# Kernel tuning notes

Hardware: AMD Instinct MI355X
Metric: run time of the kernel (lower is better)

Reference implementation:

```python
import jax, jax.numpy as jnp
import numpy as np

B, S, D, H, DK, DV = 4, 1024, 1024, 16, 64, 64
NEG = jnp.float32(-1e10)


def setup_inputs() -> dict:
    key = jax.random.key(0)
    ks = jax.random.split(key, 9)
    q = jax.random.normal(ks[0], (B, S, D), dtype=jnp.float32)
    k = jax.random.normal(ks[1], (B, S, D), dtype=jnp.float32)
    v = jax.random.normal(ks[2], (B, S, D), dtype=jnp.float32)
    pad_mask_1 = jax.random.randint(ks[3], (B,), 1, S + 1, dtype=jnp.int32)
    pad_mask_2 = jax.random.randint(ks[4], (B,), 1, S + 1, dtype=jnp.int32)
    # Per-head projection weights stacked over heads (torch Linear, bias=False).
    sc = 1.0 / np.sqrt(D)
    Wq = jax.random.uniform(ks[5], (H, D, DK), jnp.float32, -sc, sc)
    Wk = jax.random.uniform(ks[6], (H, D, DK), jnp.float32, -sc, sc)
    Wv = jax.random.uniform(ks[7], (H, D, DV), jnp.float32, -sc, sc)
    Wo = jax.random.uniform(ks[8], (H * DV, D), jnp.float32, -sc, sc)
    return {"q": q, "k": k, "v": v, "pad_mask_1": pad_mask_1,
            "pad_mask_2": pad_mask_2, "Wq": Wq, "Wk": Wk, "Wv": Wv, "Wo": Wo}


def reference(q, k, v, pad_mask_1, pad_mask_2, Wq, Wk, Wv, Wo):
    Bq, Sq, _ = q.shape
    scale = jnp.sqrt(jnp.float32(Wq.shape[-1]))
    qh = jnp.einsum('bsd,hdk->bhsk', q, Wq)   # [B,H,S,DK]
    kh = jnp.einsum('bsd,hdk->bhsk', k, Wk)
    vh = jnp.einsum('bsd,hdv->bhsv', v, Wv)
    w = jnp.einsum('bhqk,bhtk->bhqt', qh, kh) / scale  # [B,H,S,S]
    idx = jnp.arange(Sq)
    # pad_mask_1: mask key columns >= length; pad_mask_2: mask query rows >= length
    key_dead = idx[None, :] >= pad_mask_1[:, None]      # [B,S]
    row_dead = idx[None, :] >= pad_mask_2[:, None]      # [B,S]
    w = jnp.where(key_dead[:, None, None, :], NEG, w)
    w = jnp.where(row_dead[:, None, :, None], NEG, w)
    # causal: w.tril() + (-1e10).triu(1) == keep lower triangle, NEG strictly above
    causal = idx[None, :] > idx[:, None]                # [S,S] strictly upper
    w = jnp.where(causal[None, None], NEG, w)
    a = jax.nn.softmax(w, axis=-1)
    o = jnp.einsum('bhqt,bhtv->bhqv', a, vh)            # [B,H,S,DV]
    o = o.transpose(0, 2, 1, 3).reshape(Bq, Sq, -1)     # concat heads (head-major)
    return o @ Wo
```

## Files before the change

### kernel.cpp

```cpp
#include <hip/hip_runtime.h>

#define B_ 4
#define S_ 1024
#define D_ 1024
#define H_ 16
#define BSD (B_*S_*D_)

typedef unsigned short ushort_t;
typedef __attribute__((ext_vector_type(8))) __bf16 bf16x8;
typedef __attribute__((ext_vector_type(8))) ushort_t ushortx8;
typedef __attribute__((ext_vector_type(4))) float f32x4;

__device__ __forceinline__ ushort_t f2bf(float f) {
  union { float f; unsigned int u; } x; x.f = f;
  unsigned int r = x.u + 0x7fffu + ((x.u >> 16) & 1u);
  return (ushort_t)(r >> 16);
}

__device__ __forceinline__ void gll16(const void* g, void* l) {
  __builtin_amdgcn_global_load_lds(
      (const __attribute__((address_space(1))) unsigned int*)g,
      (__attribute__((address_space(3))) unsigned int*)l, 16, 0, 0);
}

#define PBAR() do { asm volatile("s_waitcnt lgkmcnt(0)" ::: "memory"); \
                    __builtin_amdgcn_s_barrier(); \
                    asm volatile("" ::: "memory"); } while (0)

__global__ __launch_bounds__(256) void transpose_w(
    const float* __restrict__ Wq, const float* __restrict__ Wk,
    const float* __restrict__ Wv, const float* __restrict__ Wo,
    ushort_t* __restrict__ WqT, ushort_t* __restrict__ WkT,
    ushort_t* __restrict__ WvT, ushort_t* __restrict__ WoT)
{
  __shared__ float tile[64][65];
  int blk = blockIdx.x;
  const float* src; ushort_t* dst;
  size_t sbase, dbase; int ld_src, ld_dst, r0, c0;
  if (blk < 768) {
    int tz = blk / 256;
    int rem = blk % 256; int head = rem >> 4; int kt = rem & 15;
    src = (tz == 0) ? Wq : (tz == 1) ? Wk : Wv;
    dst = (tz == 0) ? WqT : (tz == 1) ? WkT : WvT;
    sbase = (size_t)head * 1024 * 64; dbase = (size_t)head * 64 * 1024;
    ld_src = 64; ld_dst = 1024; r0 = kt * 64; c0 = 0;
  } else {
    int idx = blk - 768; src = Wo; dst = WoT;
    sbase = 0; dbase = 0; ld_src = 1024; ld_dst = 1024;
    r0 = (idx >> 4) * 64; c0 = (idx & 15) * 64;
  }
  int tid = threadIdx.x; int col = tid & 63; int rbase = tid >> 6;
  #pragma unroll
  for (int j = 0; j < 16; ++j) {
    int row = j * 4 + rbase;
    tile[row][col] = src[sbase + (size_t)(r0 + row) * ld_src + c0 + col];
  }
  __syncthreads();
  #pragma unroll
  for (int j = 0; j < 16; ++j) {
    int orow = j * 4 + rbase;
    dst[dbase + (size_t)(c0 + orow) * ld_dst + r0 + col] = f2bf(tile[col][orow]);
  }
}

__device__ __forceinline__ void gemm_pipe_f32A(
    const float* __restrict__ Af, const ushort_t* __restrict__ BT,
    ushort_t* __restrict__ Cb, int epi, int m0, int n0, int K)
{
  __shared__ __align__(16) ushort_t As[2][128 * 64];
  __shared__ __align__(16) ushort_t Bs[2][128 * 64];
  const int tid = threadIdx.x;
  const int wave = tid >> 6, lane = tid & 63;
  const int wm = wave >> 2, wn = wave & 3;

  f32x4 acc[4][2] = {};
  float4   ra0[2][2], ra1[2][2];
  ushortx8 rb0[2],    rb1[2];

  int offs[2], gofs[2];
  #pragma unroll
  for (int i = 0; i < 2; ++i) {
    int off = ((i * 8 + wave) << 10) + lane * 16;
    int row = off >> 7, cb = off & 127;
    int lcb = cb ^ ((row & 7) << 4);
    offs[i] = off;
    gofs[i] = row * K + (lcb >> 1);
  }

  auto loadAB = [&](float4 (&ar)[2][2], ushortx8 (&br)[2], int k0) {
    #pragma unroll
    for (int i = 0; i < 2; ++i) {
      const float* asrc = Af + (size_t)m0 * K + gofs[i] + k0;
      ar[i][0] = *(const float4*)(asrc);
      ar[i][1] = *(const float4*)(asrc + 4);
      br[i] = *(const ushortx8*)(BT + (size_t)n0 * K + gofs[i] + k0);
    }
  };
  auto writeAB = [&](int buf, const float4 (&ar)[2][2], const ushortx8 (&br)[2]) {
    #pragma unroll
    for (int i = 0; i < 2; ++i) {
      ushortx8 tv;
      #pragma unroll
      for (int j = 0; j < 4; ++j) {
        tv[j]     = f2bf(((const float*)&ar[i][0])[j]);
        tv[4 + j] = f2bf(((const float*)&ar[i][1])[j]);
      }
      *(ushortx8*)((char*)As[buf] + offs[i]) = tv;
      *(ushortx8*)((char*)Bs[buf] + offs[i]) = br[i];
    }
  };
  auto compute = [&](int buf) {
    #pragma unroll
    for (int kk = 0; kk < 2; ++kk) {
      bf16x8 af[4], bfr[2];
      #pragma unroll
      for (int mf = 0; mf < 4; ++mf) {
        int row = wm * 64 + mf * 16 + (lane & 15);
        int cb = kk * 64 + ((lane >> 4) << 4);
        af[mf] = *(const bf16x8*)((const char*)As[buf] + (row << 7) + (cb ^ ((row & 7) << 4)));
      }
      #pragma unroll
      for (int nf = 0; nf < 2; ++nf) {
        int row = wn * 32 + nf * 16 + (lane & 15);
        int cb = kk * 64 + ((lane >> 4) << 4);
        bfr[nf] = *(const bf16x8*)((const char*)Bs[buf] + (row << 7) + (cb ^ ((row & 7) << 4)));
      }
      #pragma unroll
      for (int mf = 0; mf < 4; ++mf)
        #pragma unroll
        for (int nf = 0; nf < 2; ++nf)
          acc[mf][nf] = __builtin_amdgcn_mfma_f32_16x16x32_bf16(af[mf], bfr[nf], acc[mf][nf], 0, 0, 0);
    }
  };

  const int nt = K >> 6;
  loadAB(ra0, rb0, 0);
  writeAB(0, ra0, rb0);
  loadAB(ra1, rb1, 64);
  PBAR();

  for (int t = 0; t < nt - 3; t += 2) {
    loadAB(ra0, rb0, (t + 2) << 6);
    __builtin_amdgcn_sched_barrier(0);
    compute(0);
    writeAB(1, ra1, rb1);
    PBAR();
    loadAB(ra1, rb1, (t + 3) << 6);
    __builtin_amdgcn_sched_barrier(0);
    compute(1);
    writeAB(0, ra0, rb0);
    PBAR();
  }
  compute(0);
  writeAB(1, ra1, rb1);
  PBAR();
  compute(1);

  #pragma unroll
  for (int mf = 0; mf < 4; ++mf) {
    #pragma unroll
    for (int nf = 0; nf < 2; ++nf) {
      #pragma unroll
      for (int r = 0; r < 4; ++r) {
        int m = m0 + wm * 64 + mf * 16 + ((lane >> 4) << 2) + r;
        int n = n0 + wn * 32 + nf * 16 + (lane & 15);
        float val = acc[mf][nf][r];
        if (epi == 0) {
          int b = m >> 10, s = m & 1023, h = n >> 6, dk = n & 63;
          Cb[((((size_t)(b * H_ + h)) << 10) + s) * 64 + dk] = f2bf(val);
        } else {
          int b = m >> 10, s = m & 1023, h = n >> 6, dv = n & 63;
          Cb[((((size_t)(b * H_ + h)) * 64 + dv) << 10) + s] = f2bf(val);
        }
      }
    }
  }
}

__device__ __forceinline__ void gemm_pipe_bf16(
    const ushort_t* __restrict__ A, const ushort_t* __restrict__ BT,
    float* __restrict__ Cf, int m0, int n0, int K)
{
  __shared__ __align__(16) ushort_t As[2][128 * 64];
  __shared__ __align__(16) ushort_t Bs[2][128 * 64];
  const int tid = threadIdx.x;
  const int wave = tid >> 6, lane = tid & 63;
  const int wm = wave >> 2, wn = wave & 3;

  f32x4 acc[4][2] = {};
  ushortx8 ra0[2], ra1[2], rb0[2], rb1[2];

  int offs[2], gofs[2];
  #pragma unroll
  for (int i = 0; i < 2; ++i) {
    int off = ((i * 8 + wave) << 10) + lane * 16;
    int row = off >> 7, cb = off & 127;
    int lcb = cb ^ ((row & 7) << 4);
    offs[i] = off;
    gofs[i] = row * K + (lcb >> 1);
  }

  auto loadAB = [&](ushortx8 (&ar)[2], ushortx8 (&br)[2], int k0) {
    #pragma unroll
    for (int i = 0; i < 2; ++i) {
      ar[i] = *(const ushortx8*)(A  + (size_t)m0 * K + gofs[i] + k0);
      br[i] = *(const ushortx8*)(BT + (size_t)n0 * K + gofs[i] + k0);
    }
  };
  auto writeAB = [&](int buf, const ushortx8 (&ar)[2], const ushortx8 (&br)[2]) {
    #pragma unroll
    for (int i = 0; i < 2; ++i) {
      *(ushortx8*)((char*)As[buf] + offs[i]) = ar[i];
      *(ushortx8*)((char*)Bs[buf] + offs[i]) = br[i];
    }
  };
  auto compute = [&](int buf) {
    #pragma unroll
    for (int kk = 0; kk < 2; ++kk) {
      bf16x8 af[4], bfr[2];
      #pragma unroll
      for (int mf = 0; mf < 4; ++mf) {
        int row = wm * 64 + mf * 16 + (lane & 15);
        int cb = kk * 64 + ((lane >> 4) << 4);
        af[mf] = *(const bf16x8*)((const char*)As[buf] + (row << 7) + (cb ^ ((row & 7) << 4)));
      }
      #pragma unroll
      for (int nf = 0; nf < 2; ++nf) {
        int row = wn * 32 + nf * 16 + (lane & 15);
        int cb = kk * 64 + ((lane >> 4) << 4);
        bfr[nf] = *(const bf16x8*)((const char*)Bs[buf] + (row << 7) + (cb ^ ((row & 7) << 4)));
      }
      #pragma unroll
      for (int mf = 0; mf < 4; ++mf)
        #pragma unroll
        for (int nf = 0; nf < 2; ++nf)
          acc[mf][nf] = __builtin_amdgcn_mfma_f32_16x16x32_bf16(af[mf], bfr[nf], acc[mf][nf], 0, 0, 0);
    }
  };

  const int nt = K >> 6;
  loadAB(ra0, rb0, 0);
  writeAB(0, ra0, rb0);
  loadAB(ra1, rb1, 64);
  PBAR();

  for (int t = 0; t < nt - 3; t += 2) {
    loadAB(ra0, rb0, (t + 2) << 6);
    __builtin_amdgcn_sched_barrier(0);
    compute(0);
    writeAB(1, ra1, rb1);
    PBAR();
    loadAB(ra1, rb1, (t + 3) << 6);
    __builtin_amdgcn_sched_barrier(0);
    compute(1);
    writeAB(0, ra0, rb0);
    PBAR();
  }
  compute(0);
  writeAB(1, ra1, rb1);
  PBAR();
  compute(1);

  #pragma unroll
  for (int mf = 0; mf < 4; ++mf) {
    #pragma unroll
    for (int nf = 0; nf < 2; ++nf) {
      #pragma unroll
      for (int r = 0; r < 4; ++r) {
        int m = m0 + wm * 64 + mf * 16 + ((lane >> 4) << 2) + r;
        int n = n0 + wn * 32 + nf * 16 + (lane & 15);
        Cf[(size_t)m * 1024 + n] = acc[mf][nf][r];
      }
    }
  }
}

__global__ __launch_bounds__(512, 4) void proj_gemm(
    const float* q, const float* k, const float* v,
    const ushort_t* WqT, const ushort_t* WkT, const ushort_t* WvT,
    ushort_t* qh, ushort_t* kh, ushort_t* vhT)
{
  int f = blockIdx.x;
  int xcd = f & 7;
  int slot = f >> 3;
  int g = xcd * 12 + (slot >> 3);
  int y = slot & 7;
  int z = g >> 5, x = g & 31;
  const float* A = (z == 0) ? q : (z == 1) ? k : v;
  const ushort_t* BT = (z == 0) ? WqT : (z == 1) ? WkT : WvT;
  ushort_t* C = (z == 0) ? qh : (z == 1) ? kh : vhT;
  gemm_pipe_f32A(A, BT, C, (z == 2) ? 1 : 0, x * 128, y * 128, 1024);
}

__global__ __launch_bounds__(512, 4) void out_gemm(
    const ushort_t* o, const ushort_t* WoT, float* out)
{
  int f = blockIdx.x;
  int xcd = f & 7;
  int slot = f >> 3;
  int x = xcd * 4 + (slot >> 3);
  int y = slot & 7;
  gemm_pipe_bf16(o, WoT, out, x * 128, y * 128, 1024);
}

__global__ __launch_bounds__(256) void meanv_kernel(
    const ushort_t* __restrict__ vhT, float* __restrict__ meanV)
{
  int row = blockIdx.x * 4 + (threadIdx.x >> 6);
  int lane = threadIdx.x & 63;
  const ushort_t* src = vhT + ((size_t)row << 10) + lane * 16;
  float s = 0.f;
  #pragma unroll
  for (int i = 0; i < 2; ++i) {
    bf16x8 v = *(const bf16x8*)(src + i * 8);
    #pragma unroll
    for (int j = 0; j < 8; ++j) s += (float)v[j];
  }
  #pragma unroll
  for (int mm = 1; mm < 64; mm <<= 1) s += __shfl_xor(s, mm);
  if (lane == 0) meanV[row] = s * (1.0f / 1024.0f);
}

__global__ __launch_bounds__(256) void attn_kernel(
    const ushort_t* __restrict__ qh, const ushort_t* __restrict__ kh,
    const ushort_t* __restrict__ vhT, const float* __restrict__ meanV,
    const int* __restrict__ pad1p, const int* __restrict__ pad2p,
    ushort_t* __restrict__ o)
{
  const int bh = blockIdx.x;
  const int b = bh >> 4, h = bh & 15;
  const int q0 = blockIdx.y << 6;
  const int pad1 = pad1p[b], pad2 = pad2p[b];
  const int tid = threadIdx.x, wave = tid >> 6, lane = tid & 63;

  if (q0 >= pad2) {
    int dv = tid & 63;
    int rw = tid >> 6;
    ushort_t mb = f2bf(meanV[(bh << 6) + dv]);
    for (int r = rw; r < 64; r += 4)
      o[(((size_t)((b << 10) + q0 + r)) << 10) + (h << 6) + dv] = mb;
    return;
  }

  __shared__ __align__(16) ushort_t Ks[64 * 64];
  __shared__ __align__(16) ushort_t Vs[64 * 64];
  __shared__ __align__(16) ushort_t Ps[4][16 * 64];

  const ushort_t* qbase = qh + ((size_t)bh << 16);
  const ushort_t* kbase = kh + ((size_t)bh << 16);
  const ushort_t* vbase = vhT + ((size_t)bh << 16);

  const int qrow = q0 + wave * 16 + (lane & 15);
  bf16x8 qf[2];
  qf[0] = *(const bf16x8*)(qbase + (size_t)qrow * 64 + ((lane >> 4) << 3));
  qf[1] = *(const bf16x8*)(qbase + (size_t)qrow * 64 + 32 + ((lane >> 4) << 3));

  f32x4 acc[4] = {};
  float mrow[4] = { -1e30f, -1e30f, -1e30f, -1e30f };
  float lrow[4] = { 0.f, 0.f, 0.f, 0.f };
  const int ribase = q0 + wave * 16 + ((lane >> 4) << 2);

  int t_hi = min(q0 + 63, min(pad2 - 1, pad1 - 1));
  int nb = (t_hi >> 6) + 1;

  for (int kb = 0; kb < nb; ++kb) {
    const int t0 = kb << 6;
    #pragma unroll
    for (int i = 0; i < 2; ++i) {
      int off = ((i * 4 + wave) << 10) + lane * 16;
      int row = off >> 7;
      int cb = off & 127;
      int lcb = cb ^ ((row & 7) << 4);
      gll16(kbase + (size_t)(t0 + row) * 64 + (lcb >> 1), (char*)Ks + off);
      gll16(vbase + ((size_t)row << 10) + t0 + (lcb >> 1), (char*)Vs + off);
    }
    __syncthreads();

    f32x4 sc[4];
    #pragma unroll
    for (int nf = 0; nf < 4; ++nf) {
      sc[nf] = (f32x4){0.f, 0.f, 0.f, 0.f};
      #pragma unroll
      for (int kk = 0; kk < 2; ++kk) {
        int trow = nf * 16 + (lane & 15);
        int cb = kk * 64 + ((lane >> 4) << 4);
        bf16x8 kf = *(const bf16x8*)((const char*)Ks + (trow << 7) + (cb ^ ((trow & 7) << 4)));
        sc[nf] = __builtin_amdgcn_mfma_f32_16x16x32_bf16(qf[kk], kf, sc[nf], 0, 0, 0);
      }
    }

    float pv[4][4];
    #pragma unroll
    for (int r = 0; r < 4; ++r) {
      const int irow = ribase + r;
      float sval[4];
      float rmax = -1e30f;
      #pragma unroll
      for (int nf = 0; nf < 4; ++nf) {
        int t = t0 + nf * 16 + (lane & 15);
        float vv = sc[nf][r] * 0.125f;
        if (t > irow || t >= pad1) vv = -1e10f;
        sval[nf] = vv;
        rmax = fmaxf(rmax, vv);
      }
      #pragma unroll
      for (int mm = 1; mm < 16; mm <<= 1) rmax = fmaxf(rmax, __shfl_xor(rmax, mm));
      float nm = fmaxf(mrow[r], rmax);
      float fscale = __expf(mrow[r] - nm);
      float rsum = 0.f;
      #pragma unroll
      for (int nf = 0; nf < 4; ++nf) {
        float p = __expf(sval[nf] - nm);
        pv[nf][r] = p;
        rsum += p;
      }
      #pragma unroll
      for (int mm = 1; mm < 16; mm <<= 1) rsum += __shfl_xor(rsum, mm);
      mrow[r] = nm;
      lrow[r] = lrow[r] * fscale + rsum;
      #pragma unroll
      for (int dvf = 0; dvf < 4; ++dvf) acc[dvf][r] *= fscale;
    }

    #pragma unroll
    for (int nf = 0; nf < 4; ++nf) {
      #pragma unroll
      for (int r = 0; r < 4; ++r) {
        int prow = ((lane >> 4) << 2) + r;
        int cbw = (nf * 16 + (lane & 15)) * 2;
        *(ushort_t*)((char*)Ps[wave] + (prow << 7) + (cbw ^ ((prow & 7) << 4))) = f2bf(pv[nf][r]);
      }
    }

    #pragma unroll
    for (int kk = 0; kk < 2; ++kk) {
      int prow = lane & 15;
      int cb = kk * 64 + ((lane >> 4) << 4);
      bf16x8 pf = *(const bf16x8*)((const char*)Ps[wave] + (prow << 7) + (cb ^ ((prow & 7) << 4)));
      #pragma unroll
      for (int dvf = 0; dvf < 4; ++dvf) {
        int vrow = dvf * 16 + (lane & 15);
        bf16x8 vfr = *(const bf16x8*)((const char*)Vs + (vrow << 7) + (cb ^ ((vrow & 7) << 4)));
        acc[dvf] = __builtin_amdgcn_mfma_f32_16x16x32_bf16(pf, vfr, acc[dvf], 0, 0, 0);
      }
    }
    __syncthreads();
  }

  #pragma unroll
  for (int dvf = 0; dvf < 4; ++dvf) {
    #pragma unroll
    for (int r = 0; r < 4; ++r) {
      int irow = ribase + r;
      int dv = dvf * 16 + (lane & 15);
      float val;
      if (irow < pad2) val = acc[dvf][r] * (1.0f / lrow[r]);
      else val = meanV[(bh << 6) + dv];
      o[(((size_t)((b << 10) + irow)) << 10) + (h << 6) + dv] = f2bf(val);
    }
  }
}

extern "C" void kernel_launch(void* const* d_in, const int* in_sizes, int n_in,
                              void* d_out, int out_size, void* d_ws, size_t ws_size,
                              hipStream_t stream) {
  (void)in_sizes; (void)n_in; (void)out_size; (void)ws_size;
  const float* q = (const float*)d_in[0];
  const float* k = (const float*)d_in[1];
  const float* v = (const float*)d_in[2];
  const int* pad1 = (const int*)d_in[3];
  const int* pad2 = (const int*)d_in[4];
  const float* Wq = (const float*)d_in[5];
  const float* Wk = (const float*)d_in[6];
  const float* Wv = (const float*)d_in[7];
  const float* Wo = (const float*)d_in[8];
  float* out = (float*)d_out;

  char* ws = (char*)d_ws;
  const size_t MB = 1u << 20;
  ushort_t* WqT = (ushort_t*)(ws + 24 * MB);
  ushort_t* WkT = (ushort_t*)(ws + 26 * MB);
  ushort_t* WvT = (ushort_t*)(ws + 28 * MB);
  ushort_t* WoT = (ushort_t*)(ws + 30 * MB);
  ushort_t* qh  = (ushort_t*)(ws + 32 * MB);
  ushort_t* kh  = (ushort_t*)(ws + 40 * MB);
  ushort_t* vhT = (ushort_t*)(ws + 48 * MB);
  ushort_t* ob  = (ushort_t*)(ws + 56 * MB);
  float* meanV  = (float*)(ws + 64 * MB);

  transpose_w<<<1024, 256, 0, stream>>>(Wq, Wk, Wv, Wo, WqT, WkT, WvT, WoT);
  proj_gemm<<<768, 512, 0, stream>>>(q, k, v, WqT, WkT, WvT, qh, kh, vhT);
  meanv_kernel<<<1024, 256, 0, stream>>>(vhT, meanV);
  attn_kernel<<<dim3(64, 16), 256, 0, stream>>>(qh, kh, vhT, meanV, pad1, pad2, ob);
  out_gemm<<<256, 512, 0, stream>>>(ob, WoT, out);
}
```

Baseline: 99.02 us.

## Shrink projection GEMM tile to 128x64, single-buffer LDS, stage B via direct-to-LDS loads

The projection GEMM is rewritten as a standalone kernel with a 128x64 output tile, twice as many blocks, a single LDS buffer and a higher occupancy bound (512 threads, 8 blocks). The weight operand is copied straight into LDS with global_load_lds instead of passing through registers, while the fp32 activations are still converted to bf16 in registers. The aim is more resident waves and lower register and LDS pressure to hide memory latency. In exchange it drops double buffering, adds two barriers per k-step, and re-reads the fp32 A operand twice as often across blocks.

```diff
diff --git a/kernel.cpp b/kernel.cpp
--- a/kernel.cpp
+++ b/kernel.cpp
@@ -63,9 +63,134 @@
   }
 }
 
-__device__ __forceinline__ void gemm_pipe_f32A(
-    const float* __restrict__ Af, const ushort_t* __restrict__ BT,
-    ushort_t* __restrict__ Cb, int epi, int m0, int n0, int K)
+__global__ __launch_bounds__(512, 8) void proj_gemm(
+    const float* __restrict__ q, const float* __restrict__ k,
+    const float* __restrict__ v,
+    const ushort_t* __restrict__ WqT, const ushort_t* __restrict__ WkT,
+    const ushort_t* __restrict__ WvT,
+    ushort_t* __restrict__ qh, ushort_t* __restrict__ kh,
+    ushort_t* __restrict__ vhT)
+{
+  const int f = blockIdx.x;
+  const int xcd = f & 7;
+  const int slot = f >> 3;
+  const int combo = xcd * 12 + (slot >> 4);
+  const int y = slot & 15;
+  const int z = combo >> 5, x = combo & 31;
+  const float* Af = (z == 0) ? q : (z == 1) ? k : v;
+  const ushort_t* BT = (z == 0) ? WqT : (z == 1) ? WkT : WvT;
+  ushort_t* Cb = (z == 0) ? qh : (z == 1) ? kh : vhT;
+  const int epi = (z == 2) ? 1 : 0;
+  const int m0 = x * 128, n0 = y * 64;
+  const int K = 1024;
+
+  __shared__ __align__(16) ushort_t As[128 * 64];
+  __shared__ __align__(16) ushort_t Bs[64 * 64];
+  const int tid = threadIdx.x;
+  const int wave = tid >> 6, lane = tid & 63;
+  const int wm = wave >> 1, wn = wave & 1;
+
+  f32x4 acc[2][2] = {};
+  float4 ra[2][2];
+
+  int offA[2], gofA[2];
+  #pragma unroll
+  for (int i = 0; i < 2; ++i) {
+    int off = ((i * 8 + wave) << 10) + lane * 16;
+    int row = off >> 7, cb = off & 127;
+    int lcb = cb ^ ((row & 7) << 4);
+    offA[i] = off; gofA[i] = row * K + (lcb >> 1);
+  }
+  const int offB = (wave << 10) + lane * 16;
+  const int rowB = offB >> 7, cbB = offB & 127;
+  const int gofB = rowB * K + ((cbB ^ ((rowB & 7) << 4)) >> 1);
+
+  auto loadA = [&](int k0) {
+    #pragma unroll
+    for (int i = 0; i < 2; ++i) {
+      const float* s = Af + (size_t)m0 * K + gofA[i] + k0;
+      ra[i][0] = *(const float4*)(s);
+      ra[i][1] = *(const float4*)(s + 4);
+    }
+  };
+  auto writeA = [&]() {
+    #pragma unroll
+    for (int i = 0; i < 2; ++i) {
+      ushortx8 tv;
+      #pragma unroll
+      for (int j = 0; j < 4; ++j) {
+        tv[j]     = f2bf(((const float*)&ra[i][0])[j]);
+        tv[4 + j] = f2bf(((const float*)&ra[i][1])[j]);
+      }
+      *(ushortx8*)((char*)As + offA[i]) = tv;
+    }
+  };
+  auto stageB = [&](int k0) {
+    gll16(BT + (size_t)n0 * K + gofB + k0, (char*)Bs + offB);
+  };
+  auto compute = [&]() {
+    #pragma unroll
+    for (int kk = 0; kk < 2; ++kk) {
+      bf16x8 af[2], bfr[2];
+      #pragma unroll
+      for (int mf = 0; mf < 2; ++mf) {
+        int row = wm * 32 + mf * 16 + (lane & 15);
+        int cb = kk * 64 + ((lane >> 4) << 4);
+        af[mf] = *(const bf16x8*)((const char*)As + (row << 7) + (cb ^ ((row & 7) << 4)));
+      }
+      #pragma unroll
+      for (int nf = 0; nf < 2; ++nf) {
+        int row = wn * 32 + nf * 16 + (lane & 15);
+        int cb = kk * 64 + ((lane >> 4) << 4);
+        bfr[nf] = *(const bf16x8*)((const char*)Bs + (row << 7) + (cb ^ ((row & 7) << 4)));
+      }
+      #pragma unroll
+      for (int mf = 0; mf < 2; ++mf)
+        #pragma unroll
+        for (int nf = 0; nf < 2; ++nf)
+          acc[mf][nf] = __builtin_amdgcn_mfma_f32_16x16x32_bf16(af[mf], bfr[nf], acc[mf][nf], 0, 0, 0);
+    }
+  };
+
+  loadA(0);
+  stageB(0);
+  writeA();
+  __syncthreads();
+
+  for (int t = 0; t < 15; ++t) {
+    loadA((t + 1) << 6);
+    compute();
+    __syncthreads();
+    writeA();
+    stageB((t + 1) << 6);
+    __syncthreads();
+  }
+  compute();
+
+  #pragma unroll
+  for (int mf = 0; mf < 2; ++mf) {
+    #pragma unroll
+    for (int nf = 0; nf < 2; ++nf) {
+      #pragma unroll
+      for (int r = 0; r < 4; ++r) {
+        int m = m0 + wm * 32 + mf * 16 + ((lane >> 4) << 2) + r;
+        int n = n0 + wn * 32 + nf * 16 + (lane & 15);
+        float val = acc[mf][nf][r];
+        if (epi == 0) {
+          int b = m >> 10, s = m & 1023, h = n >> 6, dk = n & 63;
+          Cb[((((size_t)(b * H_ + h)) << 10) + s) * 64 + dk] = f2bf(val);
+        } else {
+          int b = m >> 10, s = m & 1023, h = n >> 6, dv = n & 63;
+          Cb[((((size_t)(b * H_ + h)) * 64 + dv) << 10) + s] = f2bf(val);
+        }
+      }
+    }
+  }
+}
+
+__device__ __forceinline__ void gemm_pipe_bf16(
+    const ushort_t* __restrict__ A, const ushort_t* __restrict__ BT,
+    float* __restrict__ Cf, int m0, int n0, int K)
 {
   __shared__ __align__(16) ushort_t As[2][128 * 64];
   __shared__ __align__(16) ushort_t Bs[2][128 * 64];
@@ -74,8 +199,7 @@
   const int wm = wave >> 2, wn = wave & 3;
 
   f32x4 acc[4][2] = {};
-  float4   ra0[2][2], ra1[2][2];
-  ushortx8 rb0[2],    rb1[2];
+  ushortx8 ra0[2], ra1[2], rb0[2], rb1[2];
 
   int offs[2], gofs[2];
   #pragma unroll
@@ -87,25 +211,17 @@
     gofs[i] = row * K + (lcb >> 1);
   }
 
-  auto loadAB = [&](float4 (&ar)[2][2], ushortx8 (&br)[2], int k0) {
+  auto loadAB = [&](ushortx8 (&ar)[2], ushortx8 (&br)[2], int k0) {
     #pragma unroll
     for (int i = 0; i < 2; ++i) {
-      const float* asrc = Af + (size_t)m0 * K + gofs[i] + k0;
-      ar[i][0] = *(const float4*)(asrc);
-      ar[i][1] = *(const float4*)(asrc + 4);
+      ar[i] = *(const ushortx8*)(A  + (size_t)m0 * K + gofs[i] + k0);
       br[i] = *(const ushortx8*)(BT + (size_t)n0 * K + gofs[i] + k0);
     }
   };
-  auto writeAB = [&](int buf, const float4 (&ar)[2][2], const ushortx8 (&br)[2]) {
+  auto writeAB = [&](int buf, const ushortx8 (&ar)[2], const ushortx8 (&br)[2]) {
     #pragma unroll
     for (int i = 0; i < 2; ++i) {
-      ushortx8 tv;
-      #pragma unroll
-      for (int j = 0; j < 4; ++j) {
-        tv[j]     = f2bf(((const float*)&ar[i][0])[j]);
-        tv[4 + j] = f2bf(((const float*)&ar[i][1])[j]);
-      }
-      *(ushortx8*)((char*)As[buf] + offs[i]) = tv;
+      *(ushortx8*)((char*)As[buf] + offs[i]) = ar[i];
       *(ushortx8*)((char*)Bs[buf] + offs[i]) = br[i];
     }
   };
@@ -164,132 +280,10 @@
       for (int r = 0; r < 4; ++r) {
         int m = m0 + wm * 64 + mf * 16 + ((lane >> 4) << 2) + r;
         int n = n0 + wn * 32 + nf * 16 + (lane & 15);
-        float val = acc[mf][nf][r];
-        if (epi == 0) {
-          int b = m >> 10, s = m & 1023, h = n >> 6, dk = n & 63;
-          Cb[((((size_t)(b * H_ + h)) << 10) + s) * 64 + dk] = f2bf(val);
-        } else {
-          int b = m >> 10, s = m & 1023, h = n >> 6, dv = n & 63;
-          Cb[((((size_t)(b * H_ + h)) * 64 + dv) << 10) + s] = f2bf(val);
-        }
-      }
-    }
-  }
-}
-
-__device__ __forceinline__ void gemm_pipe_bf16(
-    const ushort_t* __restrict__ A, const ushort_t* __restrict__ BT,
-    float* __restrict__ Cf, int m0, int n0, int K)
-{
-  __shared__ __align__(16) ushort_t As[2][128 * 64];
-  __shared__ __align__(16) ushort_t Bs[2][128 * 64];
-  const int tid = threadIdx.x;
-  const int wave = tid >> 6, lane = tid & 63;
-  const int wm = wave >> 2, wn = wave & 3;
-
-  f32x4 acc[4][2] = {};
-  ushortx8 ra0[2], ra1[2], rb0[2], rb1[2];
-
-  int offs[2], gofs[2];
-  #pragma unroll
-  for (int i = 0; i < 2; ++i) {
-    int off = ((i * 8 + wave) << 10) + lane * 16;
-    int row = off >> 7, cb = off & 127;
-    int lcb = cb ^ ((row & 7) << 4);
-    offs[i] = off;
-    gofs[i] = row * K + (lcb >> 1);
-  }
-
-  auto loadAB = [&](ushortx8 (&ar)[2], ushortx8 (&br)[2], int k0) {
-    #pragma unroll
-    for (int i = 0; i < 2; ++i) {
-      ar[i] = *(const ushortx8*)(A  + (size_t)m0 * K + gofs[i] + k0);
-      br[i] = *(const ushortx8*)(BT + (size_t)n0 * K + gofs[i] + k0);
-    }
-  };
-  auto writeAB = [&](int buf, const ushortx8 (&ar)[2], const ushortx8 (&br)[2]) {
-    #pragma unroll
-    for (int i = 0; i < 2; ++i) {
-      *(ushortx8*)((char*)As[buf] + offs[i]) = ar[i];
-      *(ushortx8*)((char*)Bs[buf] + offs[i]) = br[i];
-    }
-  };
-  auto compute = [&](int buf) {
-    #pragma unroll
-    for (int kk = 0; kk < 2; ++kk) {
-      bf16x8 af[4], bfr[2];
-      #pragma unroll
-      for (int mf = 0; mf < 4; ++mf) {
-        int row = wm * 64 + mf * 16 + (lane & 15);
-        int cb = kk * 64 + ((lane >> 4) << 4);
-        af[mf] = *(const bf16x8*)((const char*)As[buf] + (row << 7) + (cb ^ ((row & 7) << 4)));
-      }
-      #pragma unroll
-      for (int nf = 0; nf < 2; ++nf) {
-        int row = wn * 32 + nf * 16 + (lane & 15);
-        int cb = kk * 64 + ((lane >> 4) << 4);
-        bfr[nf] = *(const bf16x8*)((const char*)Bs[buf] + (row << 7) + (cb ^ ((row & 7) << 4)));
-      }
-      #pragma unroll
-      for (int mf = 0; mf < 4; ++mf)
-        #pragma unroll
-        for (int nf = 0; nf < 2; ++nf)
-          acc[mf][nf] = __builtin_amdgcn_mfma_f32_16x16x32_bf16(af[mf], bfr[nf], acc[mf][nf], 0, 0, 0);
-    }
-  };
-
-  const int nt = K >> 6;
-  loadAB(ra0, rb0, 0);
-  writeAB(0, ra0, rb0);
-  loadAB(ra1, rb1, 64);
-  PBAR();
-
-  for (int t = 0; t < nt - 3; t += 2) {
-    loadAB(ra0, rb0, (t + 2) << 6);
-    __builtin_amdgcn_sched_barrier(0);
-    compute(0);
-    writeAB(1, ra1, rb1);
-    PBAR();
-    loadAB(ra1, rb1, (t + 3) << 6);
-    __builtin_amdgcn_sched_barrier(0);
-    compute(1);
-    writeAB(0, ra0, rb0);
-    PBAR();
-  }
-  compute(0);
-  writeAB(1, ra1, rb1);
-  PBAR();
-  compute(1);
-
-  #pragma unroll
-  for (int mf = 0; mf < 4; ++mf) {
-    #pragma unroll
-    for (int nf = 0; nf < 2; ++nf) {
-      #pragma unroll
-      for (int r = 0; r < 4; ++r) {
-        int m = m0 + wm * 64 + mf * 16 + ((lane >> 4) << 2) + r;
-        int n = n0 + wn * 32 + nf * 16 + (lane & 15);
         Cf[(size_t)m * 1024 + n] = acc[mf][nf][r];
       }
     }
   }
-}
-
-__global__ __launch_bounds__(512, 4) void proj_gemm(
-    const float* q, const float* k, const float* v,
-    const ushort_t* WqT, const ushort_t* WkT, const ushort_t* WvT,
-    ushort_t* qh, ushort_t* kh, ushort_t* vhT)
-{
-  int f = blockIdx.x;
-  int xcd = f & 7;
-  int slot = f >> 3;
-  int g = xcd * 12 + (slot >> 3);
-  int y = slot & 7;
-  int z = g >> 5, x = g & 31;
-  const float* A = (z == 0) ? q : (z == 1) ? k : v;
-  const ushort_t* BT = (z == 0) ? WqT : (z == 1) ? WkT : WvT;
-  ushort_t* C = (z == 0) ? qh : (z == 1) ? kh : vhT;
-  gemm_pipe_f32A(A, BT, C, (z == 2) ? 1 : 0, x * 128, y * 128, 1024);
 }
 
 __global__ __launch_bounds__(512, 4) void out_gemm(
@@ -489,7 +483,7 @@
   float* meanV  = (float*)(ws + 64 * MB);
 
   transpose_w<<<1024, 256, 0, stream>>>(Wq, Wk, Wv, Wo, WqT, WkT, WvT, WoT);
-  proj_gemm<<<768, 512, 0, stream>>>(q, k, v, WqT, WkT, WvT, qh, kh, vhT);
+  proj_gemm<<<1536, 512, 0, stream>>>(q, k, v, WqT, WkT, WvT, qh, kh, vhT);
   meanv_kernel<<<1024, 256, 0, stream>>>(vhT, meanV);
   attn_kernel<<<dim3(64, 16), 256, 0, stream>>>(qh, kh, vhT, meanV, pad1, pad2, ob);
   out_gemm<<<256, 512, 0, stream>>>(ob, WoT, out);
```

Measured after the change: 111.2 us. +12.3%, slower.
